# Kernel optimization log

Measured on AMD Instinct MI355X. Metric: run time of the kernel, lower is better.

The kernel has to match this reference:

```python
import jax, jax.numpy as jnp
import numpy as np

NUM_EXPERTS = 8
TOP_K = 2

def setup_inputs() -> dict:
    key = jax.random.key(0)
    k1, k2, k3, k4 = jax.random.split(key, 4)
    B, T, C, F = 4, 2048, 1024, 4096
    x = jax.random.normal(k1, (B, T, C), dtype=jnp.float32)
    gate_w = jax.random.normal(k2, (C, NUM_EXPERTS), dtype=jnp.float32) * 0.02
    w1 = jax.random.normal(k3, (NUM_EXPERTS, C, F), dtype=jnp.float32) * 0.02
    w2 = jax.random.normal(k4, (NUM_EXPERTS, F, C), dtype=jnp.float32) * 0.02
    return {"x": x, "gate_w": gate_w, "w1": w1, "w2": w2}

def reference(x, gate_w, w1, w2):
    # Router: softmax over experts, then top-k and renormalize
    router_logits = jnp.einsum('btc,ce->bte', x, gate_w)          # [B,T,E]
    routing = jax.nn.softmax(router_logits, axis=-1)
    topw, topi = jax.lax.top_k(routing, TOP_K)                    # [B,T,K]
    topw = topw / jnp.sum(topw, axis=-1, keepdims=True)
    # Combined per-expert weight per token (zero if not selected)
    onehot = jax.nn.one_hot(topi, NUM_EXPERTS, dtype=x.dtype)     # [B,T,K,E]
    combine = jnp.einsum('btk,btke->bte', topw, onehot)           # [B,T,E]
    # Expert FFNs (exact GELU, matching torch nn.GELU default)
    out = jnp.zeros_like(x)
    for e in range(NUM_EXPERTS):
        h = jax.nn.gelu(jnp.einsum('btc,cf->btf', x, w1[e]), approximate=False)
        y = jnp.einsum('btf,fc->btc', h, w2[e])
        out = out + combine[..., e:e+1] * y
    return out
```

## Files before the change

kernel.cpp:

```cpp
#include <hip/hip_runtime.h>
#include <hip/hip_bf16.h>
#include <math.h>

#define NUM_EXPERTS 8
#define NTOK 8192
#define CDIM 1024
#define FDIM 4096
#define MAXSLOTS 17408
#define MAXTILES 136
#define TILES_PER_XCD 17

typedef __bf16 bf16x8 __attribute__((ext_vector_type(8)));
typedef float  f32x4  __attribute__((ext_vector_type(4)));

#define GPTR(p) ((const __attribute__((address_space(1))) unsigned int*)(p))
#define LPTR(p) ((__attribute__((address_space(3))) unsigned int*)(p))

__device__ __forceinline__ float gelu_exact(float v){
  return 0.5f * v * (1.0f + erff(v * 0.70710678118654752f));
}

__global__ __launch_bounds__(256) void moe_router(
    const float* __restrict__ x, const float* __restrict__ gw,
    int2* __restrict__ topi, float2* __restrict__ topw, int* __restrict__ counts)
{
  int token = blockIdx.x * 4 + (threadIdx.x >> 6);
  int lane  = threadIdx.x & 63;
  int e = lane & 7, part = lane >> 3;
  const float* xr = x + (size_t)token * CDIM;
  float s = 0.f;
  int c0 = part * 128;
  for (int c = c0; c < c0 + 128; ++c) s += xr[c] * gw[c * 8 + e];
  s += __shfl_xor(s, 8); s += __shfl_xor(s, 16); s += __shfl_xor(s, 32);
  float m1 = s; int i1 = e;
  for (int off = 1; off < 8; off <<= 1){
    float ov = __shfl_xor(m1, off); int oi = __shfl_xor(i1, off);
    if (ov > m1 || (ov == m1 && oi < i1)){ m1 = ov; i1 = oi; }
  }
  float l2 = (e == i1) ? -INFINITY : s;
  float m2 = l2; int i2 = e;
  for (int off = 1; off < 8; off <<= 1){
    float ov = __shfl_xor(m2, off); int oi = __shfl_xor(i2, off);
    if (ov > m2 || (ov == m2 && oi < i2)){ m2 = ov; i2 = oi; }
  }
  if (lane == 0){
    float r = expf(m2 - m1);
    float wa = 1.f / (1.f + r);
    topi[token] = make_int2(i1, i2);
    topw[token] = make_float2(wa, 1.f - wa);
    atomicAdd(&counts[i1], 1);
    atomicAdd(&counts[i2], 1);
  }
}

__global__ __launch_bounds__(256) void convert_x_kernel(
    const float* __restrict__ x, __hip_bfloat16* __restrict__ xb)
{
  int i = (blockIdx.x * 256 + threadIdx.x) * 4;
  float4 v = *(const float4*)(x + i);
  union { __hip_bfloat16 hh[4]; ushort4 u; } cv;
  cv.hh[0] = __float2bfloat16(v.x);
  cv.hh[1] = __float2bfloat16(v.y);
  cv.hh[2] = __float2bfloat16(v.z);
  cv.hh[3] = __float2bfloat16(v.w);
  *(ushort4*)(xb + i) = cv.u;
}

__global__ __launch_bounds__(256) void transpose_bf16_kernel(
    const float* __restrict__ in, __hip_bfloat16* __restrict__ outp, int R, int Cc)
{
  __shared__ float tile[32][33];
  const size_t msz = (size_t)R * Cc;
  const float* inm = in + (size_t)blockIdx.z * msz;
  __hip_bfloat16* outm = outp + (size_t)blockIdx.z * msz;
  int r0 = blockIdx.y * 32, c0 = blockIdx.x * 32;
  int tx = threadIdx.x, ty = threadIdx.y;
  for (int yy = 0; yy < 32; yy += 8)
    tile[ty + yy][tx] = inm[(size_t)(r0 + ty + yy) * Cc + c0 + tx];
  __syncthreads();
  for (int yy = 0; yy < 32; yy += 8)
    outm[(size_t)(c0 + ty + yy) * R + r0 + tx] = __float2bfloat16(tile[tx][ty + yy]);
}

__global__ void scan_kernel(const int* __restrict__ counts, int* cursors, int* num_tiles,
    int* tile_expert, int* tile_slotbase, int* slot_token, float* slot_weight)
{
  int t = threadIdx.x;
  if (t == 0){
    int base = 0, T = 0;
    for (int e = 0; e < NUM_EXPERTS; ++e){
      cursors[e] = base;
      int nt = (counts[e] + 127) >> 7;
      for (int i = 0; i < nt; ++i){ tile_expert[T] = e; tile_slotbase[T] = base + i * 128; ++T; }
      base += nt << 7;
    }
    *num_tiles = T;
  }
  for (int i = t; i < MAXSLOTS; i += 256){ slot_token[i] = 0; slot_weight[i] = 0.f; }
}

__global__ void assign_kernel(const int2* __restrict__ topi, const float2* __restrict__ topw,
    int* cursors, int* slot_token, float* slot_weight)
{
  int token = blockIdx.x * 256 + threadIdx.x;
  int2 ii = topi[token];
  float2 ww = topw[token];
  int p0 = atomicAdd(&cursors[ii.x], 1);
  slot_token[p0] = token; slot_weight[p0] = ww.x;
  int p1 = atomicAdd(&cursors[ii.y], 1);
  slot_token[p1] = token; slot_weight[p1] = ww.y;
}

__global__ __launch_bounds__(256) void gemm1_kernel(
    const __hip_bfloat16* __restrict__ xbf, const __hip_bfloat16* __restrict__ w1t,
    __hip_bfloat16* __restrict__ h, const int* __restrict__ num_tiles,
    const int* __restrict__ tile_expert, const int* __restrict__ tile_slotbase,
    const int* __restrict__ slot_token)
{
  __shared__ __align__(16) __hip_bfloat16 As[128 * 64];
  __shared__ __align__(16) __hip_bfloat16 Bs[128 * 64];
  const int L = blockIdx.x;
  const int xcd = L & 7;
  const int j = L >> 3;
  const int tl = j >> 5;
  const int nb = j & 31;
  const int tm = xcd * TILES_PER_XCD + tl;
  if (tm >= *num_tiles) return;
  const int e = tile_expert[tm];
  const int sbase = tile_slotbase[tm];
  const int n0 = nb * 128;
  const int t = threadIdx.x;
  const int cl = t & 7;
  const __hip_bfloat16* w1e = w1t + (size_t)e * FDIM * CDIM;
  const __hip_bfloat16* aptr[4];
  const __hip_bfloat16* bptr[4];
#pragma unroll
  for (int jj = 0; jj < 4; ++jj){
    int r = jj * 32 + (t >> 3);
    int cg = cl ^ (r & 7);
    int tok = slot_token[sbase + r];
    aptr[jj] = xbf + (size_t)tok * CDIM + cg * 8;
    bptr[jj] = w1e + (size_t)(n0 + r) * CDIM + cg * 8;
  }
  char* asml = (char*)As + t * 16;
  char* bsml = (char*)Bs + t * 16;

  f32x4 acc[4][4] = {};
  const int lane = t & 63, wv = t >> 6;
  const int wm = (wv >> 1) * 64, wn = (wv & 1) * 64;
  const int lrow = lane & 15, quad = lane >> 4;

  for (int k0 = 0; k0 < CDIM; k0 += 64){
    __syncthreads();
#pragma unroll
    for (int jj = 0; jj < 4; ++jj){
      __builtin_amdgcn_global_load_lds(GPTR(aptr[jj] + k0), LPTR(asml + jj * 4096), 16, 0, 0);
      __builtin_amdgcn_global_load_lds(GPTR(bptr[jj] + k0), LPTR(bsml + jj * 4096), 16, 0, 0);
    }
    __syncthreads();
#pragma unroll
    for (int kk = 0; kk < 2; ++kk){
      bf16x8 af[4], bfr[4];
#pragma unroll
      for (int i = 0; i < 4; ++i){
        int ar = wm + i * 16 + lrow;
        int ac = (kk * 4 + quad) ^ (ar & 7);
        af[i] = *(const bf16x8*)((const char*)As + ar * 128 + ac * 16);
        int br = wn + i * 16 + lrow;
        int bc = (kk * 4 + quad) ^ (br & 7);
        bfr[i] = *(const bf16x8*)((const char*)Bs + br * 128 + bc * 16);
      }
#pragma unroll
      for (int i = 0; i < 4; ++i)
#pragma unroll
        for (int jj = 0; jj < 4; ++jj)
          acc[i][jj] = __builtin_amdgcn_mfma_f32_16x16x32_bf16(af[i], bfr[jj], acc[i][jj], 0, 0, 0);
    }
  }
#pragma unroll
  for (int i = 0; i < 4; ++i){
#pragma unroll
    for (int r = 0; r < 4; ++r){
      int row = wm + i * 16 + quad * 4 + r;
      __hip_bfloat16* hrow = h + (size_t)(sbase + row) * FDIM + n0 + wn;
#pragma unroll
      for (int jj = 0; jj < 4; ++jj)
        hrow[jj * 16 + lrow] = __float2bfloat16(gelu_exact(acc[i][jj][r]));
    }
  }
}

__global__ __launch_bounds__(256) void gemm2_kernel(
    const __hip_bfloat16* __restrict__ h, const __hip_bfloat16* __restrict__ w2t,
    float* __restrict__ out, const int* __restrict__ num_tiles,
    const int* __restrict__ tile_expert, const int* __restrict__ tile_slotbase,
    const int* __restrict__ slot_token, const float* __restrict__ slot_weight)
{
  __shared__ __align__(16) __hip_bfloat16 As[128 * 64];
  __shared__ __align__(16) __hip_bfloat16 Bs[128 * 64];
  const int L = blockIdx.x;
  const int xcd = L & 7;
  const int j = L >> 3;
  const int tl = j >> 4;
  const int nb = (j >> 1) & 7;
  const int ks = j & 1;
  const int tm = xcd * TILES_PER_XCD + tl;
  if (tm >= *num_tiles) return;
  const int e = tile_expert[tm];
  const int sbase = tile_slotbase[tm];
  const int n0 = nb * 128;
  const int t = threadIdx.x;
  const int cl = t & 7;
  const __hip_bfloat16* w2e = w2t + (size_t)e * CDIM * FDIM;
  const __hip_bfloat16* aptr[4];
  const __hip_bfloat16* bptr[4];
#pragma unroll
  for (int jj = 0; jj < 4; ++jj){
    int r = jj * 32 + (t >> 3);
    int cg = cl ^ (r & 7);
    aptr[jj] = h   + (size_t)(sbase + r) * FDIM + cg * 8;
    bptr[jj] = w2e + (size_t)(n0 + r)   * FDIM + cg * 8;
  }
  char* asml = (char*)As + t * 16;
  char* bsml = (char*)Bs + t * 16;

  f32x4 acc[4][4] = {};
  const int lane = t & 63, wv = t >> 6;
  const int wm = (wv >> 1) * 64, wn = (wv & 1) * 64;
  const int lrow = lane & 15, quad = lane >> 4;

  const int kbeg = ks * (FDIM / 2);
  for (int k0 = kbeg; k0 < kbeg + FDIM / 2; k0 += 64){
    __syncthreads();
#pragma unroll
    for (int jj = 0; jj < 4; ++jj){
      __builtin_amdgcn_global_load_lds(GPTR(aptr[jj] + k0), LPTR(asml + jj * 4096), 16, 0, 0);
      __builtin_amdgcn_global_load_lds(GPTR(bptr[jj] + k0), LPTR(bsml + jj * 4096), 16, 0, 0);
    }
    __syncthreads();
#pragma unroll
    for (int kk = 0; kk < 2; ++kk){
      bf16x8 af[4], bfr[4];
#pragma unroll
      for (int i = 0; i < 4; ++i){
        int ar = wm + i * 16 + lrow;
        int ac = (kk * 4 + quad) ^ (ar & 7);
        af[i] = *(const bf16x8*)((const char*)As + ar * 128 + ac * 16);
        int br = wn + i * 16 + lrow;
        int bc = (kk * 4 + quad) ^ (br & 7);
        bfr[i] = *(const bf16x8*)((const char*)Bs + br * 128 + bc * 16);
      }
#pragma unroll
      for (int i = 0; i < 4; ++i)
#pragma unroll
        for (int jj = 0; jj < 4; ++jj)
          acc[i][jj] = __builtin_amdgcn_mfma_f32_16x16x32_bf16(af[i], bfr[jj], acc[i][jj], 0, 0, 0);
    }
  }
#pragma unroll
  for (int i = 0; i < 4; ++i){
#pragma unroll
    for (int r = 0; r < 4; ++r){
      int row = wm + i * 16 + quad * 4 + r;
      int slot = sbase + row;
      int tok = slot_token[slot];
      float wgt = slot_weight[slot];
      float* orow = out + (size_t)tok * CDIM + n0 + wn;
#pragma unroll
      for (int jj = 0; jj < 4; ++jj)
        atomicAdd(&orow[jj * 16 + lrow], wgt * acc[i][jj][r]);
    }
  }
}

__global__ __launch_bounds__(256) void naive_kernel(
    const float* __restrict__ x, const float* __restrict__ w1, const float* __restrict__ w2,
    const int2* __restrict__ topi, const float2* __restrict__ topw, float* __restrict__ out)
{
  __shared__ float xs[CDIM];
  __shared__ float hs[FDIM];
  int token = blockIdx.x;
  int t = threadIdx.x;
  for (int i = t; i < CDIM; i += 256) xs[i] = x[(size_t)token * CDIM + i];
  float acc[4] = {0.f, 0.f, 0.f, 0.f};
  int2 ei = topi[token]; float2 ew = topw[token];
  int elist[2] = {ei.x, ei.y}; float wlist[2] = {ew.x, ew.y};
  for (int kk = 0; kk < 2; ++kk){
    int e = elist[kk]; float wgt = wlist[kk];
    __syncthreads();
    for (int f = t; f < FDIM; f += 256){
      const float* wcol = w1 + (size_t)e * CDIM * FDIM + f;
      float s = 0.f;
      for (int c = 0; c < CDIM; ++c) s += xs[c] * wcol[(size_t)c * FDIM];
      hs[f] = gelu_exact(s);
    }
    __syncthreads();
    for (int ii = 0; ii < 4; ++ii){
      int c = ii * 256 + t;
      const float* w2col = w2 + (size_t)e * FDIM * CDIM + c;
      float s = 0.f;
      for (int f = 0; f < FDIM; ++f) s += hs[f] * w2col[(size_t)f * CDIM];
      acc[ii] += wgt * s;
    }
  }
  for (int ii = 0; ii < 4; ++ii) out[(size_t)token * CDIM + ii * 256 + t] = acc[ii];
}

extern "C" void kernel_launch(void* const* d_in, const int* in_sizes, int n_in,
                              void* d_out, int out_size, void* d_ws, size_t ws_size,
                              hipStream_t stream)
{
  const float* x  = (const float*)d_in[0];
  const float* gw = (const float*)d_in[1];
  const float* w1 = (const float*)d_in[2];
  const float* w2 = (const float*)d_in[3];
  float* out = (float*)d_out;
  char* ws = (char*)d_ws;

  int*    counts        = (int*)(ws + 0);
  int*    cursors       = (int*)(ws + 32);
  int*    num_tiles     = (int*)(ws + 64);
  int*    tile_expert   = (int*)(ws + 256);
  int*    tile_slotbase = (int*)(ws + 1024);
  int2*   topi          = (int2*)(ws + 4096);
  float2* topw          = (float2*)(ws + 4096 + 65536);
  int*    slot_token    = (int*)(ws + 135168);
  float*  slot_weight   = (float*)(ws + 204800);
  const size_t XBF_OFF = 1u << 20;
  const size_t W1T_OFF = XBF_OFF + (size_t)NTOK * CDIM * 2;
  const size_t W2T_OFF = W1T_OFF + (size_t)NUM_EXPERTS * CDIM * FDIM * 2;
  const size_t H_OFF   = W2T_OFF + (size_t)NUM_EXPERTS * CDIM * FDIM * 2;
  const size_t NEED    = H_OFF + (size_t)MAXSLOTS * FDIM * 2;
  __hip_bfloat16* xbf = (__hip_bfloat16*)(ws + XBF_OFF);
  __hip_bfloat16* w1t = (__hip_bfloat16*)(ws + W1T_OFF);
  __hip_bfloat16* w2t = (__hip_bfloat16*)(ws + W2T_OFF);
  __hip_bfloat16* h   = (__hip_bfloat16*)(ws + H_OFF);

  hipMemsetAsync(ws, 0, 4096, stream);
  hipMemsetAsync(d_out, 0, (size_t)out_size * sizeof(float), stream);

  moe_router<<<NTOK / 4, 256, 0, stream>>>(x, gw, topi, topw, counts);

  if (ws_size >= NEED){
    convert_x_kernel<<<NTOK * CDIM / (4 * 256), 256, 0, stream>>>(x, xbf);
    transpose_bf16_kernel<<<dim3(FDIM / 32, CDIM / 32, NUM_EXPERTS), dim3(32, 8), 0, stream>>>(w1, w1t, CDIM, FDIM);
    transpose_bf16_kernel<<<dim3(CDIM / 32, FDIM / 32, NUM_EXPERTS), dim3(32, 8), 0, stream>>>(w2, w2t, FDIM, CDIM);
    scan_kernel<<<1, 256, 0, stream>>>(counts, cursors, num_tiles, tile_expert, tile_slotbase, slot_token, slot_weight);
    assign_kernel<<<NTOK / 256, 256, 0, stream>>>(topi, topw, cursors, slot_token, slot_weight);
    gemm1_kernel<<<8 * TILES_PER_XCD * 32, 256, 0, stream>>>(xbf, w1t, h, num_tiles, tile_expert, tile_slotbase, slot_token);
    gemm2_kernel<<<8 * TILES_PER_XCD * 8 * 2, 256, 0, stream>>>(h, w2t, out, num_tiles, tile_expert, tile_slotbase, slot_token, slot_weight);
  } else {
    naive_kernel<<<NTOK, 256, 0, stream>>>(x, w1, w2, topi, topw, out);
  }
}
```

Before: 1.210 ms.

## Replace atomic scatter with per-slot expert output and gather-combine kernel

GEMM2 no longer split-K's and scatters with fp32 atomics into the output. It writes bf16 per-slot results into a scratch buffer, reusing the w1t region since gemm1 has already finished with it. A new combine kernel gathers each token's two slots and writes the weighted sum, which removes the output memset and the atomic contention. Both GEMM epilogues now stage tiles through swizzled LDS for coalesced 16-byte stores, and the weight transpose uses 64x64 tiles with vectorized float4 loads and bf16 LDS. The trade-offs are halving GEMM2's grid parallelism by dropping split-K, an extra bf16 rounding of the expert outputs, and one extra kernel launch.

```diff
diff --git a/kernel.cpp b/kernel.cpp
--- a/kernel.cpp
+++ b/kernel.cpp
@@ -18,6 +18,9 @@
 
 __device__ __forceinline__ float gelu_exact(float v){
   return 0.5f * v * (1.0f + erff(v * 0.70710678118654752f));
+}
+__device__ __forceinline__ float bf2f(unsigned short u){
+  union { unsigned int i; float f; } cv; cv.i = ((unsigned int)u) << 16; return cv.f;
 }
 
 __global__ __launch_bounds__(256) void moe_router(
@@ -69,17 +72,34 @@
 __global__ __launch_bounds__(256) void transpose_bf16_kernel(
     const float* __restrict__ in, __hip_bfloat16* __restrict__ outp, int R, int Cc)
 {
-  __shared__ float tile[32][33];
+  __shared__ __hip_bfloat16 tile[64 * 66];
   const size_t msz = (size_t)R * Cc;
   const float* inm = in + (size_t)blockIdx.z * msz;
   __hip_bfloat16* outm = outp + (size_t)blockIdx.z * msz;
-  int r0 = blockIdx.y * 32, c0 = blockIdx.x * 32;
-  int tx = threadIdx.x, ty = threadIdx.y;
-  for (int yy = 0; yy < 32; yy += 8)
-    tile[ty + yy][tx] = inm[(size_t)(r0 + ty + yy) * Cc + c0 + tx];
+  int r0 = blockIdx.y * 64, c0 = blockIdx.x * 64;
+  int t = threadIdx.x;
+  int r = t & 63, cseg = (t >> 6) * 16;
+  const float* src = inm + (size_t)(r0 + r) * Cc + c0 + cseg;
+  float4 v0 = ((const float4*)src)[0];
+  float4 v1 = ((const float4*)src)[1];
+  float4 v2 = ((const float4*)src)[2];
+  float4 v3 = ((const float4*)src)[3];
+  float vv[16] = {v0.x,v0.y,v0.z,v0.w, v1.x,v1.y,v1.z,v1.w,
+                  v2.x,v2.y,v2.z,v2.w, v3.x,v3.y,v3.z,v3.w};
+#pragma unroll
+  for (int k = 0; k < 16; ++k)
+    tile[(cseg + k) * 66 + r] = __float2bfloat16(vv[k]);
   __syncthreads();
-  for (int yy = 0; yy < 32; yy += 8)
-    outm[(size_t)(c0 + ty + yy) * R + r0 + tx] = __float2bfloat16(tile[tx][ty + yy]);
+#pragma unroll
+  for (int p = 0; p < 2; ++p){
+    int cc = p * 32 + (t >> 3), ch = (t & 7) * 8;
+    const unsigned short* rowp = (const unsigned short*)tile + cc * 66 + ch;
+    unsigned int a = *(const unsigned int*)(rowp + 0);
+    unsigned int b = *(const unsigned int*)(rowp + 2);
+    unsigned int c = *(const unsigned int*)(rowp + 4);
+    unsigned int d = *(const unsigned int*)(rowp + 6);
+    *(uint4*)(outm + (size_t)(c0 + cc) * R + r0 + ch) = make_uint4(a, b, c, d);
+  }
 }
 
 __global__ void scan_kernel(const int* __restrict__ counts, int* cursors, int* num_tiles,
@@ -100,7 +120,7 @@
 }
 
 __global__ void assign_kernel(const int2* __restrict__ topi, const float2* __restrict__ topw,
-    int* cursors, int* slot_token, float* slot_weight)
+    int* cursors, int* slot_token, float* slot_weight, int2* __restrict__ token_slots)
 {
   int token = blockIdx.x * 256 + threadIdx.x;
   int2 ii = topi[token];
@@ -109,6 +129,7 @@
   slot_token[p0] = token; slot_weight[p0] = ww.x;
   int p1 = atomicAdd(&cursors[ii.y], 1);
   slot_token[p1] = token; slot_weight[p1] = ww.y;
+  token_slots[token] = make_int2(p0, p1);
 }
 
 __global__ __launch_bounds__(256) void gemm1_kernel(
@@ -117,8 +138,7 @@
     const int* __restrict__ tile_expert, const int* __restrict__ tile_slotbase,
     const int* __restrict__ slot_token)
 {
-  __shared__ __align__(16) __hip_bfloat16 As[128 * 64];
-  __shared__ __align__(16) __hip_bfloat16 Bs[128 * 64];
+  __shared__ __align__(16) char smem[32768];
   const int L = blockIdx.x;
   const int xcd = L & 7;
   const int j = L >> 3;
@@ -142,8 +162,8 @@
     aptr[jj] = xbf + (size_t)tok * CDIM + cg * 8;
     bptr[jj] = w1e + (size_t)(n0 + r) * CDIM + cg * 8;
   }
-  char* asml = (char*)As + t * 16;
-  char* bsml = (char*)Bs + t * 16;
+  char* asml = smem + t * 16;
+  char* bsml = smem + 16384 + t * 16;
 
   f32x4 acc[4][4] = {};
   const int lane = t & 63, wv = t >> 6;
@@ -165,10 +185,10 @@
       for (int i = 0; i < 4; ++i){
         int ar = wm + i * 16 + lrow;
         int ac = (kk * 4 + quad) ^ (ar & 7);
-        af[i] = *(const bf16x8*)((const char*)As + ar * 128 + ac * 16);
+        af[i] = *(const bf16x8*)(smem + ar * 128 + ac * 16);
         int br = wn + i * 16 + lrow;
         int bc = (kk * 4 + quad) ^ (br & 7);
-        bfr[i] = *(const bf16x8*)((const char*)Bs + br * 128 + bc * 16);
+        bfr[i] = *(const bf16x8*)(smem + 16384 + br * 128 + bc * 16);
       }
 #pragma unroll
       for (int i = 0; i < 4; ++i)
@@ -177,33 +197,42 @@
           acc[i][jj] = __builtin_amdgcn_mfma_f32_16x16x32_bf16(af[i], bfr[jj], acc[i][jj], 0, 0, 0);
     }
   }
-#pragma unroll
-  for (int i = 0; i < 4; ++i){
+  __syncthreads();
+  __hip_bfloat16* Ct = (__hip_bfloat16*)smem;
+#pragma unroll
+  for (int i = 0; i < 4; ++i)
 #pragma unroll
     for (int r = 0; r < 4; ++r){
       int row = wm + i * 16 + quad * 4 + r;
-      __hip_bfloat16* hrow = h + (size_t)(sbase + row) * FDIM + n0 + wn;
-#pragma unroll
-      for (int jj = 0; jj < 4; ++jj)
-        hrow[jj * 16 + lrow] = __float2bfloat16(gelu_exact(acc[i][jj][r]));
-    }
+#pragma unroll
+      for (int jj = 0; jj < 4; ++jj){
+        int col = wn + jj * 16 + lrow;
+        int cc = (col >> 3) ^ (row & 15);
+        Ct[row * 128 + cc * 8 + (col & 7)] = __float2bfloat16(gelu_exact(acc[i][jj][r]));
+      }
+    }
+  __syncthreads();
+#pragma unroll
+  for (int v = 0; v < 8; ++v){
+    int Lr = v * 256 + t;
+    int row = Lr >> 4, cc = Lr & 15;
+    int cs = cc ^ (row & 15);
+    uint4 val = *(const uint4*)(Ct + row * 128 + cs * 8);
+    *(uint4*)(h + (size_t)(sbase + row) * FDIM + n0 + cc * 8) = val;
   }
 }
 
 __global__ __launch_bounds__(256) void gemm2_kernel(
     const __hip_bfloat16* __restrict__ h, const __hip_bfloat16* __restrict__ w2t,
-    float* __restrict__ out, const int* __restrict__ num_tiles,
-    const int* __restrict__ tile_expert, const int* __restrict__ tile_slotbase,
-    const int* __restrict__ slot_token, const float* __restrict__ slot_weight)
-{
-  __shared__ __align__(16) __hip_bfloat16 As[128 * 64];
-  __shared__ __align__(16) __hip_bfloat16 Bs[128 * 64];
+    __hip_bfloat16* __restrict__ y, const int* __restrict__ num_tiles,
+    const int* __restrict__ tile_expert, const int* __restrict__ tile_slotbase)
+{
+  __shared__ __align__(16) char smem[32768];
   const int L = blockIdx.x;
   const int xcd = L & 7;
   const int j = L >> 3;
-  const int tl = j >> 4;
-  const int nb = (j >> 1) & 7;
-  const int ks = j & 1;
+  const int tl = j >> 3;
+  const int nb = j & 7;
   const int tm = xcd * TILES_PER_XCD + tl;
   if (tm >= *num_tiles) return;
   const int e = tile_expert[tm];
@@ -221,16 +250,15 @@
     aptr[jj] = h   + (size_t)(sbase + r) * FDIM + cg * 8;
     bptr[jj] = w2e + (size_t)(n0 + r)   * FDIM + cg * 8;
   }
-  char* asml = (char*)As + t * 16;
-  char* bsml = (char*)Bs + t * 16;
+  char* asml = smem + t * 16;
+  char* bsml = smem + 16384 + t * 16;
 
   f32x4 acc[4][4] = {};
   const int lane = t & 63, wv = t >> 6;
   const int wm = (wv >> 1) * 64, wn = (wv & 1) * 64;
   const int lrow = lane & 15, quad = lane >> 4;
 
-  const int kbeg = ks * (FDIM / 2);
-  for (int k0 = kbeg; k0 < kbeg + FDIM / 2; k0 += 64){
+  for (int k0 = 0; k0 < FDIM; k0 += 64){
     __syncthreads();
 #pragma unroll
     for (int jj = 0; jj < 4; ++jj){
@@ -245,10 +273,10 @@
       for (int i = 0; i < 4; ++i){
         int ar = wm + i * 16 + lrow;
         int ac = (kk * 4 + quad) ^ (ar & 7);
-        af[i] = *(const bf16x8*)((const char*)As + ar * 128 + ac * 16);
+        af[i] = *(const bf16x8*)(smem + ar * 128 + ac * 16);
         int br = wn + i * 16 + lrow;
         int bc = (kk * 4 + quad) ^ (br & 7);
-        bfr[i] = *(const bf16x8*)((const char*)Bs + br * 128 + bc * 16);
+        bfr[i] = *(const bf16x8*)(smem + 16384 + br * 128 + bc * 16);
       }
 #pragma unroll
       for (int i = 0; i < 4; ++i)
@@ -257,20 +285,47 @@
           acc[i][jj] = __builtin_amdgcn_mfma_f32_16x16x32_bf16(af[i], bfr[jj], acc[i][jj], 0, 0, 0);
     }
   }
-#pragma unroll
-  for (int i = 0; i < 4; ++i){
+  __syncthreads();
+  __hip_bfloat16* Ct = (__hip_bfloat16*)smem;
+#pragma unroll
+  for (int i = 0; i < 4; ++i)
 #pragma unroll
     for (int r = 0; r < 4; ++r){
       int row = wm + i * 16 + quad * 4 + r;
-      int slot = sbase + row;
-      int tok = slot_token[slot];
-      float wgt = slot_weight[slot];
-      float* orow = out + (size_t)tok * CDIM + n0 + wn;
-#pragma unroll
-      for (int jj = 0; jj < 4; ++jj)
-        atomicAdd(&orow[jj * 16 + lrow], wgt * acc[i][jj][r]);
-    }
-  }
+#pragma unroll
+      for (int jj = 0; jj < 4; ++jj){
+        int col = wn + jj * 16 + lrow;
+        int cc = (col >> 3) ^ (row & 15);
+        Ct[row * 128 + cc * 8 + (col & 7)] = __float2bfloat16(acc[i][jj][r]);
+      }
+    }
+  __syncthreads();
+#pragma unroll
+  for (int v = 0; v < 8; ++v){
+    int Lr = v * 256 + t;
+    int row = Lr >> 4, cc = Lr & 15;
+    int cs = cc ^ (row & 15);
+    uint4 val = *(const uint4*)(Ct + row * 128 + cs * 8);
+    *(uint4*)(y + (size_t)(sbase + row) * CDIM + n0 + cc * 8) = val;
+  }
+}
+
+__global__ __launch_bounds__(256) void combine_kernel(
+    const __hip_bfloat16* __restrict__ y, const int2* __restrict__ token_slots,
+    const float* __restrict__ slot_weight, float* __restrict__ out)
+{
+  int token = blockIdx.x;
+  int c = threadIdx.x * 4;
+  int2 ss = token_slots[token];
+  float w0 = slot_weight[ss.x], w1 = slot_weight[ss.y];
+  ushort4 a = *(const ushort4*)((const unsigned short*)y + (size_t)ss.x * CDIM + c);
+  ushort4 b = *(const ushort4*)((const unsigned short*)y + (size_t)ss.y * CDIM + c);
+  float4 o;
+  o.x = w0 * bf2f(a.x) + w1 * bf2f(b.x);
+  o.y = w0 * bf2f(a.y) + w1 * bf2f(b.y);
+  o.z = w0 * bf2f(a.z) + w1 * bf2f(b.z);
+  o.w = w0 * bf2f(a.w) + w1 * bf2f(b.w);
+  *(float4*)(out + (size_t)token * CDIM + c) = o;
 }
 
 __global__ __launch_bounds__(256) void naive_kernel(
@@ -323,9 +378,10 @@
   int*    tile_expert   = (int*)(ws + 256);
   int*    tile_slotbase = (int*)(ws + 1024);
   int2*   topi          = (int2*)(ws + 4096);
-  float2* topw          = (float2*)(ws + 4096 + 65536);
+  float2* topw          = (float2*)(ws + 69632);
   int*    slot_token    = (int*)(ws + 135168);
   float*  slot_weight   = (float*)(ws + 204800);
+  int2*   token_slots   = (int2*)(ws + 278528);
   const size_t XBF_OFF = 1u << 20;
   const size_t W1T_OFF = XBF_OFF + (size_t)NTOK * CDIM * 2;
   const size_t W2T_OFF = W1T_OFF + (size_t)NUM_EXPERTS * CDIM * FDIM * 2;
@@ -335,20 +391,21 @@
   __hip_bfloat16* w1t = (__hip_bfloat16*)(ws + W1T_OFF);
   __hip_bfloat16* w2t = (__hip_bfloat16*)(ws + W2T_OFF);
   __hip_bfloat16* h   = (__hip_bfloat16*)(ws + H_OFF);
+  __hip_bfloat16* y   = (__hip_bfloat16*)(ws + W1T_OFF);
 
   hipMemsetAsync(ws, 0, 4096, stream);
-  hipMemsetAsync(d_out, 0, (size_t)out_size * sizeof(float), stream);
 
   moe_router<<<NTOK / 4, 256, 0, stream>>>(x, gw, topi, topw, counts);
 
   if (ws_size >= NEED){
     convert_x_kernel<<<NTOK * CDIM / (4 * 256), 256, 0, stream>>>(x, xbf);
-    transpose_bf16_kernel<<<dim3(FDIM / 32, CDIM / 32, NUM_EXPERTS), dim3(32, 8), 0, stream>>>(w1, w1t, CDIM, FDIM);
-    transpose_bf16_kernel<<<dim3(CDIM / 32, FDIM / 32, NUM_EXPERTS), dim3(32, 8), 0, stream>>>(w2, w2t, FDIM, CDIM);
+    transpose_bf16_kernel<<<dim3(FDIM / 64, CDIM / 64, NUM_EXPERTS), 256, 0, stream>>>(w1, w1t, CDIM, FDIM);
+    transpose_bf16_kernel<<<dim3(CDIM / 64, FDIM / 64, NUM_EXPERTS), 256, 0, stream>>>(w2, w2t, FDIM, CDIM);
     scan_kernel<<<1, 256, 0, stream>>>(counts, cursors, num_tiles, tile_expert, tile_slotbase, slot_token, slot_weight);
-    assign_kernel<<<NTOK / 256, 256, 0, stream>>>(topi, topw, cursors, slot_token, slot_weight);
+    assign_kernel<<<NTOK / 256, 256, 0, stream>>>(topi, topw, cursors, slot_token, slot_weight, token_slots);
     gemm1_kernel<<<8 * TILES_PER_XCD * 32, 256, 0, stream>>>(xbf, w1t, h, num_tiles, tile_expert, tile_slotbase, slot_token);
-    gemm2_kernel<<<8 * TILES_PER_XCD * 8 * 2, 256, 0, stream>>>(h, w2t, out, num_tiles, tile_expert, tile_slotbase, slot_token, slot_weight);
+    gemm2_kernel<<<8 * TILES_PER_XCD * 8, 256, 0, stream>>>(h, w2t, y, num_tiles, tile_expert, tile_slotbase);
+    combine_kernel<<<NTOK, 256, 0, stream>>>(y, token_slots, slot_weight, out);
   } else {
     naive_kernel<<<NTOK, 256, 0, stream>>>(x, w1, w2, topi, topw, out);
   }
```

New measurement: 1.136 ms. -6.2%, faster.
